# Performance work log

Measured on AMD Instinct MI355X. Metric: run time of the kernel, lower is better.

Reference implementation:

```python
import jax, jax.numpy as jnp
import numpy as np

NEG_SLOPE = 0.2  # GATConv default negative_slope


def gat_conv(x, row, col, W, b, a_src, a_dst, N):
    # GATConv, heads=1, flow='target_to_source': i=row (central), j=col (neighbor)
    h = x @ W                                                   # [N, C]
    e = jax.nn.leaky_relu((h @ a_src)[col] + (h @ a_dst)[row], NEG_SLOPE)  # [E]
    m = jax.ops.segment_max(e, row, num_segments=N)             # segment softmax over row
    w = jnp.exp(e - m[row])
    denom = jax.ops.segment_sum(w, row, num_segments=N)
    alpha = w / (denom[row] + 1e-16)
    out = jax.ops.segment_sum(alpha[:, None] * h[col], row, num_segments=N)
    return out + b


def lstm_scan(xs_t, Wih, Whh, bih, bhh):
    # xs_t: [L, N, C] -> hidden states [L, N, H]; PyTorch gate order i,f,g,o
    H = Whh.shape[1]
    Nn = xs_t.shape[1]
    bias = bih + bhh
    def step(carry, xt):
        h, c = carry
        g = xt @ Wih.T + h @ Whh.T + bias
        i, f, gg, o = jnp.split(g, 4, axis=-1)
        c = jax.nn.sigmoid(f) * c + jax.nn.sigmoid(i) * jnp.tanh(gg)
        h = jax.nn.sigmoid(o) * jnp.tanh(c)
        return (h, c), h
    init = (jnp.zeros((Nn, H), xs_t.dtype), jnp.zeros((Nn, H), xs_t.dtype))
    _, hs = jax.lax.scan(step, init, xs_t)
    return hs


def jk_lstm(xst, Wih_f, Whh_f, bih_f, bhh_f, Wih_b, Whh_b, bih_b, bhh_b, att_W, att_b):
    # xst: [L, N, C]; bidirectional LSTM over layer dim, attention-weighted sum
    hf = lstm_scan(xst, Wih_f, Whh_f, bih_f, bhh_f)
    hb = lstm_scan(xst[::-1], Wih_b, Whh_b, bih_b, bhh_b)[::-1]
    h = jnp.concatenate([hf, hb], axis=-1)                      # [L, N, 2H]
    score = jnp.einsum('lnh,h->ln', h, att_W) + att_b           # [L, N]
    alpha = jax.nn.softmax(score, axis=0)                       # softmax over layers
    return jnp.einsum('lnc,ln->nc', xst, alpha)                 # [N, C]


def setup_inputs() -> dict:
    key = jax.random.key(0)
    ks = list(jax.random.split(key, 32))
    N, E, C = 50000, 800000, 128
    L = 3
    H = (L * C) // 2  # 192; PyG JumpingKnowledge lstm hidden size
    s = 0.05
    d = {}
    d['x'] = jax.random.normal(ks[0], (N, 3), jnp.float32)
    d['edge_index'] = jax.random.randint(ks[1], (2, E), 0, N, jnp.int64)
    d['gat_W0'] = jax.random.normal(ks[2], (3, C)) * 0.3
    d['gat_b0'] = jnp.zeros((C,))
    d['gat_as0'] = jax.random.normal(ks[3], (C,)) * s
    d['gat_ad0'] = jax.random.normal(ks[4], (C,)) * s
    d['gat_W'] = jax.random.normal(ks[5], (L - 1, C, C)) * s
    d['gat_b'] = jnp.zeros((L - 1, C))
    d['gat_as'] = jax.random.normal(ks[6], (L - 1, C)) * s
    d['gat_ad'] = jax.random.normal(ks[7], (L - 1, C)) * s
    d['lstm_Wih_f'] = jax.random.normal(ks[8], (4 * H, C)) * s
    d['lstm_Whh_f'] = jax.random.normal(ks[9], (4 * H, H)) * s
    d['lstm_bih_f'] = jnp.zeros((4 * H,))
    d['lstm_bhh_f'] = jnp.zeros((4 * H,))
    d['lstm_Wih_b'] = jax.random.normal(ks[10], (4 * H, C)) * s
    d['lstm_Whh_b'] = jax.random.normal(ks[11], (4 * H, H)) * s
    d['lstm_bih_b'] = jnp.zeros((4 * H,))
    d['lstm_bhh_b'] = jnp.zeros((4 * H,))
    d['att_W'] = jax.random.normal(ks[12], (2 * H,)) * s
    d['att_b'] = jnp.zeros((1,))
    d['nW1'] = jax.random.normal(ks[13], (C, C)) * s
    d['nb1'] = jnp.zeros((C,))
    d['nW2'] = jax.random.normal(ks[14], (C, 2)) * s
    d['nb2'] = jnp.zeros((2,))
    d['eW1'] = jax.random.normal(ks[15], (2 * C, C)) * s
    d['eb1'] = jnp.zeros((C,))
    d['eW2'] = jax.random.normal(ks[16], (C, 2)) * s
    d['eb2'] = jnp.zeros((2,))
    return d


def reference(x, edge_index, gat_W0, gat_b0, gat_as0, gat_ad0, gat_W, gat_b, gat_as, gat_ad,
              lstm_Wih_f, lstm_Whh_f, lstm_bih_f, lstm_bhh_f,
              lstm_Wih_b, lstm_Whh_b, lstm_bih_b, lstm_bhh_b,
              att_W, att_b, nW1, nb1, nW2, nb2, eW1, eb1, eW2, eb2):
    N = x.shape[0]
    row, col = edge_index[0], edge_index[1]
    xs = []
    h = jax.nn.relu(gat_conv(x, row, col, gat_W0, gat_b0, gat_as0, gat_ad0, N))
    xs.append(h)
    for l in range(gat_W.shape[0]):  # fixed small layer count
        h = jax.nn.relu(gat_conv(h, row, col, gat_W[l], gat_b[l], gat_as[l], gat_ad[l], N))
        xs.append(h)
    xst = jnp.stack(xs, axis=0)  # [L, N, C]
    h = jk_lstm(xst, lstm_Wih_f, lstm_Whh_f, lstm_bih_f, lstm_bhh_f,
                lstm_Wih_b, lstm_Whh_b, lstm_bih_b, lstm_bhh_b, att_W, att_b)
    # node classifier (dropout is identity in eval)
    node_out = jax.nn.softmax(jax.nn.relu(h @ nW1 + nb1) @ nW2 + nb2, axis=1)
    # edge representation gather + concat, then edge classifier
    edge_rep = jnp.concatenate([h[row], h[col]], axis=1)  # [E, 2C]
    edge_out = jax.nn.softmax(jax.nn.relu(edge_rep @ eW1 + eb1) @ eW2 + eb2, axis=1)
    return node_out, edge_out
```

## Files before the change

kernel.cpp:

```cpp
#include <hip/hip_runtime.h>
#include <cstdint>
#include <cstddef>


#define NIN 28
#define MAXJOBS 20

struct InPtrs { const void* p[NIN]; int n[NIN]; };

struct PrepCfg {
    const void* src[MAXJOBS];
    float* dst[MAXJOBS];
    int n[MAXJOBS];
    int ai[MAXJOBS];
    int blk0[MAXJOBS + 1];
    int njobs;
    int cvB, wB, gB, tB;
    const void* esrc; int* row; int* col; int* cnt; int E;
    const void *Wihf, *Whhf, *Wihb, *Whhb, *bihf, *bhhf, *bihb, *bhhb;
    unsigned short* Bpack; float* bsum;
    const void* Wgsrc; unsigned short* Wg;
    const void* nW1src; const void* eW1src; unsigned short* Wt;
};

typedef short s16x4 __attribute__((ext_vector_type(4)));
typedef short s16x8 __attribute__((ext_vector_type(8)));
typedef float f32x4 __attribute__((ext_vector_type(4)));
typedef unsigned short u16x8 __attribute__((ext_vector_type(8)));

__device__ __forceinline__ float bf2f(unsigned short v) {
    unsigned int u = ((unsigned int)v) << 16;
    return __uint_as_float(u);
}

__device__ __forceinline__ unsigned short f2bf(float x) {
    unsigned int u = __float_as_uint(x);
    unsigned int r = u + 0x7fffu + ((u >> 16) & 1u);
    return (unsigned short)(r >> 16);
}

__device__ __forceinline__ float rdx(const void* p, size_t i, int isf32) {
    return isf32 ? ((const float*)p)[i] : bf2f(((const unsigned short*)p)[i]);
}

__device__ __forceinline__ float frcp(float x) {
    return __builtin_amdgcn_rcpf(x);
}

__device__ __forceinline__ float sigm(float x) {
    return frcp(1.f + __expf(-x));
}

__device__ __forceinline__ float fast_tanh(float x) {
    return 1.f - 2.f * frcp(__expf(2.f * x) + 1.f);
}

__global__ void k_sniff(InPtrs in, int* flags) {
    int ai = blockIdx.x;
    if (ai >= NIN) return;
    __shared__ int cnt;
    if (threadIdx.x == 0) cnt = 0;
    __syncthreads();
    if (ai == 1) {
        const int* w = (const int*)in.p[1];
        int nw = in.n[1] < 512 ? in.n[1] : 512;
        int local = 0;
        for (int i = threadIdx.x; i < nw; i += blockDim.x)
            if ((i & 1) && w[i] != 0) local++;
        atomicAdd(&cnt, local);
        __syncthreads();
        if (threadIdx.x == 0) flags[1] = (cnt < 4) ? 1 : 0;
        return;
    }
    const unsigned short* u = (const unsigned short*)in.p[ai];
    int ns = in.n[ai] < 256 ? in.n[ai] : 256;
    int local = 0;
    for (int i = threadIdx.x; i < ns; i += blockDim.x) {
        if (i & 1) continue;
        unsigned short v = u[i];
        int e = (v >> 7) & 0xff;
        if ((v & 0x7fff) != 0 && (e < 100 || e > 154)) local++;
    }
    atomicAdd(&cnt, local);
    __syncthreads();
    if (threadIdx.x == 0) flags[ai] = (cnt * 4 >= ns) ? 1 : 0;
}

__global__ void k_prep(PrepCfg C, const int* __restrict__ flags) {
    const int b = blockIdx.x;
    const int tid = threadIdx.x;
    if (b < C.cvB) {
        int j = 0;
        while (j + 1 < C.njobs && b >= C.blk0[j + 1]) ++j;
        int i = (b - C.blk0[j]) * 256 + tid;
        if (i < C.n[j]) C.dst[j][i] = rdx(C.src[j], i, flags[C.ai[j]]);
        return;
    }
    if (b < C.wB) {
        int i = (b - C.cvB) * 256 + tid;
        if (i >= C.E) return;
        int r, c;
        if (flags[1]) {
            const long long* s = (const long long*)C.esrc;
            r = (int)s[i];
            c = (int)s[(size_t)C.E + i];
        } else {
            const int* s = (const int*)C.esrc;
            r = s[i];
            c = s[(size_t)C.E + i];
        }
        C.row[i] = r;
        C.col[i] = c;
        atomicAdd(&C.cnt[r], 1);
        return;
    }
    if (b < C.gB) {
        int idx = (b - C.wB) * 256 + tid;
        const int TOT = 2 * 10 * 48 * 512;
        if (idx < TOT) {
            int dir = idx / (10 * 48 * 512);
            int r   = idx % (10 * 48 * 512);
            int kb  = r / (48 * 512);
            int r2  = r % (48 * 512);
            int f   = r2 / 512;
            int q   = r2 % 512;
            int lane = q >> 3, j = q & 7;
            int k   = kb * 32 + ((j >> 2) * 16) + ((lane >> 4) * 4) + (j & 3);
            int col = f * 16 + (lane & 15);
            float v;
            if (k < 128)
                v = dir ? rdx(C.Wihb, (size_t)col * 128 + k, flags[14])
                        : rdx(C.Wihf, (size_t)col * 128 + k, flags[10]);
            else
                v = dir ? rdx(C.Whhb, (size_t)col * 192 + (k - 128), flags[15])
                        : rdx(C.Whhf, (size_t)col * 192 + (k - 128), flags[11]);
            C.Bpack[idx] = f2bf(v);
        }
        if (idx < 2 * 768) {
            int d = idx / 768, j = idx % 768;
            C.bsum[idx] = d ? rdx(C.bihb, j, flags[16]) + rdx(C.bhhb, j, flags[17])
                            : rdx(C.bihf, j, flags[12]) + rdx(C.bhhf, j, flags[13]);
        }
        return;
    }
    if (b < C.tB) {
        int idx = (b - C.gB) * 256 + tid;
        if (idx >= 2 * 4 * 8 * 512) return;
        int layer = idx / 16384;
        int r  = idx % 16384;
        int kb = r / 4096;
        int r2 = r % 4096;
        int f  = r2 / 512;
        int q  = r2 % 512;
        int lane = q >> 3, j = q & 7;
        int k   = kb * 32 + ((j >> 2) * 16) + ((lane >> 4) * 4) + (j & 3);
        int col = f * 16 + (lane & 15);
        C.Wg[idx] = f2bf(rdx(C.Wgsrc, (size_t)layer * 16384 + (size_t)k * 128 + col,
                             flags[6]));
        return;
    }
    {
        int idx = (b - C.tB) * 256 + tid;
        if (idx >= 4 * 24 * 512) return;
        int kb = idx / (24 * 512);
        int r  = idx % (24 * 512);
        int fr = r / 512;
        int q  = r % 512;
        int lane = q >> 3, j = q & 7;
        int k   = kb * 32 + ((j >> 2) * 16) + ((lane >> 4) * 4) + (j & 3);
        int grp = fr >> 3;
        int col = (fr & 7) * 16 + (lane & 15);
        float v;
        if (grp == 0)      v = rdx(C.nW1src, (size_t)k * 128 + col, flags[20]);
        else if (grp == 1) v = rdx(C.eW1src, (size_t)k * 128 + col, flags[24]);
        else               v = rdx(C.eW1src, (size_t)(128 + k) * 128 + col, flags[24]);
        C.Wt[idx] = f2bf(v);
    }
}

__global__ void k_scan1(const int* __restrict__ deg, int* __restrict__ indptr,
                        int* __restrict__ bsums, int N) {
    __shared__ int buf[1024];
    const int t = threadIdx.x;
    const int base = blockIdx.x * 1024;
    int v = (base + t < N) ? deg[base + t] : 0;
    buf[t] = v;
    __syncthreads();
    for (int ofs = 1; ofs < 1024; ofs <<= 1) {
        int add = (t >= ofs) ? buf[t - ofs] : 0;
        __syncthreads();
        buf[t] += add;
        __syncthreads();
    }
    if (base + t < N) indptr[base + t] = buf[t] - v;
    if (t == 1023) bsums[blockIdx.x] = buf[1023];
}

__global__ void k_scan2(int* bsums, int nb) {
    if (threadIdx.x == 0 && blockIdx.x == 0) {
        int acc = 0;
        for (int j = 0; j < nb; ++j) { int v = bsums[j]; bsums[j] = acc; acc += v; }
        bsums[nb] = acc;
    }
}

__global__ void k_scan3(const int* __restrict__ bsums, int* __restrict__ indptr,
                        int* __restrict__ cnt, int N, int nb) {
    int i = blockIdx.x * blockDim.x + threadIdx.x;
    if (i < N) {
        indptr[i] += bsums[i >> 10];
        cnt[i] = 0;
    }
    if (i == 0) indptr[N] = bsums[nb];
}

__global__ void k_fill(const int* __restrict__ row, const int* __restrict__ col,
                       const int* __restrict__ indptr, int* __restrict__ cur,
                       int* __restrict__ colS, int* __restrict__ eidx, int E) {
    int i = blockIdx.x * blockDim.x + threadIdx.x;
    if (i >= E) return;
    int r = row[i];
    int p = indptr[r] + atomicAdd(&cur[r], 1);
    colS[p] = col[i];
    eidx[p] = i;
}

__global__ __launch_bounds__(256) void k_lin0(
    const float* __restrict__ x, const float* __restrict__ W0,
    const float* __restrict__ asrc, const float* __restrict__ adst,
    unsigned short* __restrict__ hlin, float* __restrict__ hs, float* __restrict__ hd,
    int N) {
    const int wid = threadIdx.x >> 6, lane = threadIdx.x & 63;
    const int n = blockIdx.x * 4 + wid;
    if (n >= N) return;
    float x0 = x[(size_t)n * 3], x1 = x[(size_t)n * 3 + 1], x2 = x[(size_t)n * 3 + 2];
    const int c0 = lane, c1 = lane + 64;
    float h0 = x0 * W0[c0] + x1 * W0[128 + c0] + x2 * W0[256 + c0];
    float h1 = x0 * W0[c1] + x1 * W0[128 + c1] + x2 * W0[256 + c1];
    hlin[(size_t)n * 128 + c0] = f2bf(h0);
    hlin[(size_t)n * 128 + c1] = f2bf(h1);
    float sp = h0 * asrc[c0] + h1 * asrc[c1];
    float dp = h0 * adst[c0] + h1 * adst[c1];
    for (int o = 32; o; o >>= 1) { sp += __shfl_down(sp, o); dp += __shfl_down(dp, o); }
    if (lane == 0) { hs[n] = sp; hd[n] = dp; }
}

__global__ __launch_bounds__(512) void k_linm(
    const unsigned short* __restrict__ xin,
    const unsigned short* __restrict__ Wg,
    const float* __restrict__ asrc, const float* __restrict__ adst,
    unsigned short* __restrict__ hlin, float* __restrict__ hs, float* __restrict__ hd,
    int N) {
    __shared__ unsigned short AS[64][136];
    __shared__ float hsS[64], hdS[64];
    const int t = threadIdx.x;
    const int f = t >> 6, lane = t & 63;
    const int n0 = blockIdx.x * 64;
    const int ccol = lane & 15;
    const int klane = lane >> 4;
    const int lrow = klane * 4;
    const int akl = klane * 4;
    const int m = f * 16 + ccol;

    const float asv = asrc[m], adv = adst[m];

    for (int i = t; i < 1024; i += 512) {
        int r = i >> 4, kq = (i & 15) * 8;
        u16x8 v = (u16x8)(0);
        if (n0 + r < N) v = *(const u16x8*)(xin + (size_t)(n0 + r) * 128 + kq);
        *(u16x8*)&AS[r][kq] = v;
    }
    if (t < 64) { hsS[t] = 0.f; hdS[t] = 0.f; }
    __syncthreads();

    f32x4 acc[4];
    #pragma unroll
    for (int rf = 0; rf < 4; ++rf) acc[rf] = (f32x4)(0.f);
    #pragma unroll
    for (int kb = 0; kb < 4; ++kb) {
        s16x8 b = *(const s16x8*)(Wg + ((size_t)kb * 8 + f) * 512 + lane * 8);
        const int k0 = kb * 32 + akl;
        #pragma unroll
        for (int rf = 0; rf < 4; ++rf) {
            s16x4 alo = *(const s16x4*)&AS[rf * 16 + ccol][k0];
            s16x4 ahi = *(const s16x4*)&AS[rf * 16 + ccol][k0 + 16];
            s16x8 av = __builtin_shufflevector(alo, ahi, 0, 1, 2, 3, 4, 5, 6, 7);
            acc[rf] = __builtin_amdgcn_mfma_f32_16x16x32_bf16(av, b, acc[rf], 0, 0, 0);
        }
    }
    __syncthreads();

    float sp[16], dp[16];
    #pragma unroll
    for (int rf = 0; rf < 4; ++rf) {
        #pragma unroll
        for (int reg = 0; reg < 4; ++reg) {
            float h = acc[rf][reg];
            int ci = rf * 4 + reg;
            AS[rf * 16 + lrow + reg][m] = f2bf(h);
            sp[ci] = h * asv;
            dp[ci] = h * adv;
        }
    }
    #pragma unroll
    for (int o = 1; o < 16; o <<= 1) {
        #pragma unroll
        for (int i = 0; i < 16; ++i) { sp[i] += __shfl_xor(sp[i], o); dp[i] += __shfl_xor(dp[i], o); }
    }
    if (ccol == 0) {
        #pragma unroll
        for (int i = 0; i < 16; ++i) {
            int row = (i >> 2) * 16 + lrow + (i & 3);
            atomicAdd(&hsS[row], sp[i]);
            atomicAdd(&hdS[row], dp[i]);
        }
    }
    __syncthreads();

    for (int i = t; i < 1024; i += 512) {
        int r = i >> 4, kq = (i & 15) * 8;
        if (n0 + r < N)
            *(u16x8*)(hlin + (size_t)(n0 + r) * 128 + kq) = *(const u16x8*)&AS[r][kq];
    }
    if (t < 64 && n0 + t < N) { hs[n0 + t] = hsS[t]; hd[n0 + t] = hdS[t]; }
}

__global__ __launch_bounds__(256) void k_aggr(
    const unsigned short* __restrict__ hlin, const float* __restrict__ hs,
    const float* __restrict__ hd,
    const int* __restrict__ indptr, const int* __restrict__ colS,
    const float* __restrict__ b, unsigned short* __restrict__ xout, int N) {
    const int wid = threadIdx.x >> 6, lane = threadIdx.x & 63;
    const int n = blockIdx.x * 4 + wid;
    if (n >= N) return;
    const int s = indptr[n], epos = indptr[n + 1];
    const float hdv = hd[n];
    const int c0 = lane * 2, c1 = lane * 2 + 1;
    float m = -1e30f, d = 0.f, a0 = 0.f, a1 = 0.f;
    int idx = s;
    for (; idx + 8 <= epos; idx += 8) {
        int cl[8];
        #pragma unroll
        for (int j = 0; j < 8; ++j) cl[j] = colS[idx + j];
        float e[8];
        #pragma unroll
        for (int j = 0; j < 8; ++j) {
            float ev = hs[cl[j]] + hdv;
            e[j] = (ev > 0.f) ? ev : 0.2f * ev;
        }
        unsigned int hw[8];
        #pragma unroll
        for (int j = 0; j < 8; ++j)
            hw[j] = *(const unsigned int*)(hlin + (size_t)cl[j] * 128 + c0);
        float m8 = e[0];
        #pragma unroll
        for (int j = 1; j < 8; ++j) m8 = fmaxf(m8, e[j]);
        if (m8 > m) {
            float sc = __expf(m - m8);
            a0 *= sc; a1 *= sc; d *= sc; m = m8;
        }
        #pragma unroll
        for (int j = 0; j < 8; ++j) {
            float w = __expf(e[j] - m);
            a0 += w * bf2f((unsigned short)(hw[j] & 0xffffu));
            a1 += w * bf2f((unsigned short)(hw[j] >> 16));
            d  += w;
        }
    }
    for (; idx < epos; ++idx) {
        int col = colS[idx];
        float e = hs[col] + hdv;
        e = (e > 0.f) ? e : 0.2f * e;
        unsigned int hw = *(const unsigned int*)(hlin + (size_t)col * 128 + c0);
        float v0 = bf2f((unsigned short)(hw & 0xffffu));
        float v1 = bf2f((unsigned short)(hw >> 16));
        if (e > m) {
            float sc = __expf(m - e);
            a0 = a0 * sc + v0;
            a1 = a1 * sc + v1;
            d  = d * sc + 1.f;
            m  = e;
        } else {
            float w = __expf(e - m);
            a0 += w * v0;
            a1 += w * v1;
            d  += w;
        }
    }
    float inv = frcp(d + 1e-16f);
    float r0 = a0 * inv + b[c0];
    float r1 = a1 * inv + b[c1];
    unsigned int ow = (unsigned int)f2bf(fmaxf(r0, 0.f))
                    | ((unsigned int)f2bf(fmaxf(r1, 0.f)) << 16);
    *(unsigned int*)(xout + (size_t)n * 128 + c0) = ow;
}

__global__ __launch_bounds__(768, 3) void k_lstm_mfma(
    const unsigned short* __restrict__ xsb,
    const unsigned short* __restrict__ Bpack,
    const float* __restrict__ bsum,
    const float* __restrict__ attW,
    float* __restrict__ scoreP,
    int N) {
    __shared__ unsigned short AS[64][332];
    __shared__ float scoreS[64];
    const int t = threadIdx.x;
    const int bf = t >> 6, lane = t & 63;
    const int dir = blockIdx.y;
    const int n0 = blockIdx.x * 64;
    const int ccol = lane & 15;
    const int klane = lane >> 4;
    const int lrow = klane * 4;
    const int akl = klane * 4;
    const int m = bf * 16 + ccol;

    const float bI = bsum[dir * 768 + m];
    const float bF = bsum[dir * 768 + 192 + m];
    const float bG = bsum[dir * 768 + 384 + m];
    const float bO = bsum[dir * 768 + 576 + m];
    const float awt = attW[dir * 192 + m];
    float cst[16];
    #pragma unroll
    for (int i = 0; i < 16; ++i) cst[i] = 0.f;

    const unsigned short* Bd = Bpack + (size_t)dir * 10 * 48 * 512;

    {
        const int l0 = dir ? 2 : 0;
        const unsigned short* xsrc = xsb + ((size_t)l0 * N + n0) * 128;
        for (int i = t; i < 1024; i += 768) {
            int r = i >> 4, kq = (i & 15) * 8;
            u16x8 v = (u16x8)(0);
            if (n0 + r < N) v = *(const u16x8*)(xsrc + (size_t)r * 128 + kq);
            *(u16x8*)&AS[r][kq] = v;
        }
    }
    if (t < 64) scoreS[t] = 0.f;
    __syncthreads();

    for (int s = 0; s < 3; ++s) {
        const int l = dir ? (2 - s) : s;

        const int KB = s ? 10 : 4;
        f32x4 acc[4][4];
        #pragma unroll
        for (int rf = 0; rf < 4; ++rf)
            #pragma unroll
            for (int g = 0; g < 4; ++g) acc[rf][g] = (f32x4)(0.f);
        s16x8 bA[4], bB[4];
        {
            const unsigned short* bb = Bd + (size_t)bf * 512 + lane * 8;
            #pragma unroll
            for (int g = 0; g < 4; ++g) bA[g] = *(const s16x8*)(bb + (size_t)g * 6144);
        }
        for (int kb = 0; kb < KB; kb += 2) {
            {
                const unsigned short* bb = Bd + ((size_t)(kb + 1) * 48 + bf) * 512 + lane * 8;
                #pragma unroll
                for (int g = 0; g < 4; ++g) bB[g] = *(const s16x8*)(bb + (size_t)g * 6144);
            }
            {
                const int k0 = kb * 32 + akl;
                s16x8 av[4];
                #pragma unroll
                for (int rf = 0; rf < 4; ++rf) {
                    s16x4 alo = *(const s16x4*)&AS[rf * 16 + ccol][k0];
                    s16x4 ahi = *(const s16x4*)&AS[rf * 16 + ccol][k0 + 16];
                    av[rf] = __builtin_shufflevector(alo, ahi, 0, 1, 2, 3, 4, 5, 6, 7);
                }
                #pragma unroll
                for (int rf = 0; rf < 4; ++rf)
                    #pragma unroll
                    for (int g = 0; g < 4; ++g)
                        acc[rf][g] = __builtin_amdgcn_mfma_f32_16x16x32_bf16(
                            av[rf], bA[g], acc[rf][g], 0, 0, 0);
            }
            if (kb + 2 < KB) {
                const unsigned short* bb = Bd + ((size_t)(kb + 2) * 48 + bf) * 512 + lane * 8;
                #pragma unroll
                for (int g = 0; g < 4; ++g) bA[g] = *(const s16x8*)(bb + (size_t)g * 6144);
            }
            {
                const int k0 = (kb + 1) * 32 + akl;
                s16x8 av[4];
                #pragma unroll
                for (int rf = 0; rf < 4; ++rf) {
                    s16x4 alo = *(const s16x4*)&AS[rf * 16 + ccol][k0];
                    s16x4 ahi = *(const s16x4*)&AS[rf * 16 + ccol][k0 + 16];
                    av[rf] = __builtin_shufflevector(alo, ahi, 0, 1, 2, 3, 4, 5, 6, 7);
                }
                #pragma unroll
                for (int rf = 0; rf < 4; ++rf)
                    #pragma unroll
                    for (int g = 0; g < 4; ++g)
                        acc[rf][g] = __builtin_amdgcn_mfma_f32_16x16x32_bf16(
                            av[rf], bB[g], acc[rf][g], 0, 0, 0);
            }
        }
        __syncthreads();

        u16x8 nx0 = (u16x8)(0), nx1 = (u16x8)(0);
        if (s < 2) {
            const int ln = dir ? (1 - s) : (s + 1);
            const unsigned short* xsrc = xsb + ((size_t)ln * N + n0) * 128;
            {
                int r = t >> 4, kq = (t & 15) * 8;
                if (n0 + r < N) nx0 = *(const u16x8*)(xsrc + (size_t)r * 128 + kq);
            }
            if (t < 256) {
                int i = t + 768, r = i >> 4, kq = (i & 15) * 8;
                if (n0 + r < N) nx1 = *(const u16x8*)(xsrc + (size_t)r * 128 + kq);
            }
        }

        float sp[16];
        #pragma unroll
        for (int rf = 0; rf < 4; ++rf) {
            #pragma unroll
            for (int reg = 0; reg < 4; ++reg) {
                float gI = acc[rf][0][reg] + bI;
                float gF = acc[rf][1][reg] + bF;
                float gG = acc[rf][2][reg] + bG;
                float gO = acc[rf][3][reg] + bO;
                float ig = sigm(gI);
                float fg = sigm(gF);
                float gt = fast_tanh(gG);
                float og = sigm(gO);
                int ci = rf * 4 + reg;
                float cn = fg * cst[ci] + ig * gt;
                cst[ci] = cn;
                float hh = og * fast_tanh(cn);
                AS[rf * 16 + lrow + reg][128 + m] = f2bf(hh);
                sp[ci] = hh * awt;
            }
        }
        #pragma unroll
        for (int o = 1; o < 16; o <<= 1) {
            #pragma unroll
            for (int i = 0; i < 16; ++i) sp[i] += __shfl_xor(sp[i], o);
        }
        if (ccol == 0) {
            #pragma unroll
            for (int i = 0; i < 16; ++i)
                atomicAdd(&scoreS[(i >> 2) * 16 + lrow + (i & 3)], sp[i]);
        }

        if (s < 2) {
            {
                int r = t >> 4, kq = (t & 15) * 8;
                *(u16x8*)&AS[r][kq] = nx0;
            }
            if (t < 256) {
                int i = t + 768, r = i >> 4, kq = (i & 15) * 8;
                *(u16x8*)&AS[r][kq] = nx1;
            }
        }
        __syncthreads();

        if (t < 64) {
            if (n0 + t < N)
                scoreP[(size_t)(dir * 3 + l) * N + n0 + t] = scoreS[t];
            scoreS[t] = 0.f;
        }
    }
}

__global__ __launch_bounds__(512) void k_tailm(
    const unsigned short* __restrict__ xsb, const float* __restrict__ scoreP,
    const unsigned short* __restrict__ Wt,
    const float* __restrict__ nb1, const float* __restrict__ nW2,
    const float* __restrict__ nb2, const float* __restrict__ eb1,
    unsigned short* __restrict__ P, unsigned short* __restrict__ Q,
    float* __restrict__ out, int N) {
    __shared__ unsigned short AS[64][136];
    __shared__ float al[64][4];
    __shared__ float lgt[64][2];
    const int t = threadIdx.x;
    const int f = t >> 6, lane = t & 63;
    const int n0 = blockIdx.x * 64;
    const int ccol = lane & 15;
    const int klane = lane >> 4;
    const int lrow = klane * 4;
    const int akl = klane * 4;
    const int m = f * 16 + ccol;

    if (t < 64) {
        int n = n0 + t;
        float e0 = 0.f, e1 = 0.f, e2 = 0.f;
        if (n < N) {
            float s0 = scoreP[n]                 + scoreP[(size_t)3 * N + n];
            float s1 = scoreP[(size_t)N + n]     + scoreP[(size_t)4 * N + n];
            float s2 = scoreP[(size_t)2 * N + n] + scoreP[(size_t)5 * N + n];
            float mm = fmaxf(s0, fmaxf(s1, s2));
            e0 = __expf(s0 - mm); e1 = __expf(s1 - mm); e2 = __expf(s2 - mm);
            float inv = frcp(e0 + e1 + e2);
            e0 *= inv; e1 *= inv; e2 *= inv;
        }
        al[t][0] = e0; al[t][1] = e1; al[t][2] = e2;
        lgt[t][0] = 0.f; lgt[t][1] = 0.f;
    }
    __syncthreads();

    const size_t L1o = (size_t)N * 128, L2o = 2 * L1o;
    for (int i = t; i < 1024; i += 512) {
        int r = i >> 4, kq = (i & 15) * 8;
        u16x8 o8 = (u16x8)(0);
        if (n0 + r < N) {
            size_t base = (size_t)(n0 + r) * 128 + kq;
            u16x8 a = *(const u16x8*)(xsb + base);
            u16x8 b = *(const u16x8*)(xsb + L1o + base);
            u16x8 c = *(const u16x8*)(xsb + L2o + base);
            float w0 = al[r][0], w1 = al[r][1], w2 = al[r][2];
            #pragma unroll
            for (int j = 0; j < 8; ++j)
                o8[j] = f2bf(w0 * bf2f(a[j]) + w1 * bf2f(b[j]) + w2 * bf2f(c[j]));
        }
        *(u16x8*)&AS[r][kq] = o8;
    }
    __syncthreads();

    f32x4 accN[4], accP[4], accQ[4];
    #pragma unroll
    for (int rf = 0; rf < 4; ++rf) { accN[rf] = (f32x4)(0.f); accP[rf] = (f32x4)(0.f); accQ[rf] = (f32x4)(0.f); }
    #pragma unroll
    for (int kb = 0; kb < 4; ++kb) {
        s16x8 bN = *(const s16x8*)(Wt + ((size_t)kb * 24 + f) * 512 + lane * 8);
        s16x8 bP = *(const s16x8*)(Wt + ((size_t)kb * 24 + 8 + f) * 512 + lane * 8);
        s16x8 bQ = *(const s16x8*)(Wt + ((size_t)kb * 24 + 16 + f) * 512 + lane * 8);
        const int k0 = kb * 32 + akl;
        #pragma unroll
        for (int rf = 0; rf < 4; ++rf) {
            s16x4 alo = *(const s16x4*)&AS[rf * 16 + ccol][k0];
            s16x4 ahi = *(const s16x4*)&AS[rf * 16 + ccol][k0 + 16];
            s16x8 av = __builtin_shufflevector(alo, ahi, 0, 1, 2, 3, 4, 5, 6, 7);
            accN[rf] = __builtin_amdgcn_mfma_f32_16x16x32_bf16(av, bN, accN[rf], 0, 0, 0);
            accP[rf] = __builtin_amdgcn_mfma_f32_16x16x32_bf16(av, bP, accP[rf], 0, 0, 0);
            accQ[rf] = __builtin_amdgcn_mfma_f32_16x16x32_bf16(av, bQ, accQ[rf], 0, 0, 0);
        }
    }
    __syncthreads();

    {
        const float nb1v = nb1[m];
        const float w20 = nW2[2 * m], w21 = nW2[2 * m + 1];
        float s0[16], s1[16];
        #pragma unroll
        for (int rf = 0; rf < 4; ++rf) {
            #pragma unroll
            for (int reg = 0; reg < 4; ++reg) {
                float h = fmaxf(accN[rf][reg] + nb1v, 0.f);
                int ci = rf * 4 + reg;
                s0[ci] = h * w20;
                s1[ci] = h * w21;
            }
        }
        #pragma unroll
        for (int o = 1; o < 16; o <<= 1) {
            #pragma unroll
            for (int i = 0; i < 16; ++i) { s0[i] += __shfl_xor(s0[i], o); s1[i] += __shfl_xor(s1[i], o); }
        }
        if (ccol == 0) {
            #pragma unroll
            for (int i = 0; i < 16; ++i) {
                int row = (i >> 2) * 16 + lrow + (i & 3);
                atomicAdd(&lgt[row][0], s0[i]);
                atomicAdd(&lgt[row][1], s1[i]);
            }
        }
    }
    {
        const float eb1v = eb1[m];
        #pragma unroll
        for (int rf = 0; rf < 4; ++rf)
            #pragma unroll
            for (int reg = 0; reg < 4; ++reg)
                AS[rf * 16 + lrow + reg][m] = f2bf(accP[rf][reg] + eb1v);
    }
    __syncthreads();
    if (t < 64 && n0 + t < N) {
        float l0 = lgt[t][0] + nb2[0], l1 = lgt[t][1] + nb2[1];
        float mm = fmaxf(l0, l1);
        float e0 = __expf(l0 - mm), e1 = __expf(l1 - mm);
        float inv = frcp(e0 + e1);
        out[2 * (size_t)(n0 + t)]     = e0 * inv;
        out[2 * (size_t)(n0 + t) + 1] = e1 * inv;
    }
    for (int i = t; i < 1024; i += 512) {
        int r = i >> 4, kq = (i & 15) * 8;
        if (n0 + r < N)
            *(u16x8*)(P + (size_t)(n0 + r) * 128 + kq) = *(const u16x8*)&AS[r][kq];
    }
    __syncthreads();
    #pragma unroll
    for (int rf = 0; rf < 4; ++rf)
        #pragma unroll
        for (int reg = 0; reg < 4; ++reg)
            AS[rf * 16 + lrow + reg][m] = f2bf(accQ[rf][reg]);
    __syncthreads();
    for (int i = t; i < 1024; i += 512) {
        int r = i >> 4, kq = (i & 15) * 8;
        if (n0 + r < N)
            *(u16x8*)(Q + (size_t)(n0 + r) * 128 + kq) = *(const u16x8*)&AS[r][kq];
    }
}

__global__ __launch_bounds__(256) void k_edge3(
    const unsigned short* __restrict__ P, const unsigned short* __restrict__ Q,
    const int* __restrict__ indptr, const int* __restrict__ colS,
    const int* __restrict__ eidx,
    const float* __restrict__ W2, const float* __restrict__ b2,
    float* __restrict__ out, int N) {
    const int wid = threadIdx.x >> 6, lane = threadIdx.x & 63;
    const int n = blockIdx.x * 4 + wid;
    if (n >= N) return;
    const int sl = lane & 15, g = lane >> 4;
    const int s = indptr[n], e = indptr[n + 1];
    float pf[8];
    {
        u16x8 pv = *(const u16x8*)(P + (size_t)n * 128 + sl * 8);
        #pragma unroll
        for (int j = 0; j < 8; ++j) pf[j] = bf2f(pv[j]);
    }
    const float* W2f = W2;
    const float b20 = b2[0], b21 = b2[1];
    for (int p = s + g; p < e; p += 8) {
        int p1 = p + 4;
        bool v1 = p1 < e;
        int col0 = colS[p],  eo0 = eidx[p];
        int col1 = v1 ? colS[p1] : col0;
        int eo1  = v1 ? eidx[p1] : 0;
        u16x8 qv0 = *(const u16x8*)(Q + (size_t)col0 * 128 + sl * 8);
        u16x8 qv1 = *(const u16x8*)(Q + (size_t)col1 * 128 + sl * 8);
        float l00 = 0.f, l01 = 0.f, l10 = 0.f, l11 = 0.f;
        #pragma unroll
        for (int j = 0; j < 8; ++j) {
            int ch = sl * 8 + j;
            float wA = W2f[ch * 2], wB = W2f[ch * 2 + 1];
            float h0 = fmaxf(pf[j] + bf2f(qv0[j]), 0.f);
            float h1 = fmaxf(pf[j] + bf2f(qv1[j]), 0.f);
            l00 += h0 * wA; l01 += h0 * wB;
            l10 += h1 * wA; l11 += h1 * wB;
        }
        #pragma unroll
        for (int o = 1; o < 16; o <<= 1) {
            l00 += __shfl_xor(l00, o); l01 += __shfl_xor(l01, o);
            l10 += __shfl_xor(l10, o); l11 += __shfl_xor(l11, o);
        }
        if (sl == 0) {
            {
                float a = l00 + b20, b = l01 + b21;
                float mm = fmaxf(a, b);
                float e0 = __expf(a - mm), e1 = __expf(b - mm);
                float inv = frcp(e0 + e1);
                out[2 * (size_t)N + 2 * (size_t)eo0]     = e0 * inv;
                out[2 * (size_t)N + 2 * (size_t)eo0 + 1] = e1 * inv;
            }
            if (v1) {
                float a = l10 + b20, b = l11 + b21;
                float mm = fmaxf(a, b);
                float e0 = __expf(a - mm), e1 = __expf(b - mm);
                float inv = frcp(e0 + e1);
                out[2 * (size_t)N + 2 * (size_t)eo1]     = e0 * inv;
                out[2 * (size_t)N + 2 * (size_t)eo1 + 1] = e1 * inv;
            }
        }
    }
}

extern "C" void kernel_launch(void* const* d_in, const int* in_sizes, int n_in,
                              void* d_out, int out_size, void* d_ws, size_t ws_size,
                              hipStream_t stream) {
    if (n_in < NIN) return;
    const int N = in_sizes[0] / 3;
    const int E = in_sizes[1] / 2;

    char* ws = (char*)d_ws;
    size_t off = 0;
    auto alloc = [&](size_t bytes) -> char* {
        char* p = ws + off;
        off = (off + bytes + 255) & ~(size_t)255;
        return p;
    };
    auto skipCanon = [](int i) {
        return i == 1 || (i >= 10 && i <= 17) || i == 6 || i == 20 || i == 24;
    };
    int* flags = (int*)alloc(32 * sizeof(int));
    int* bsums = (int*)alloc(128 * sizeof(int));
    float* canon[NIN];
    for (int i = 0; i < NIN; ++i) canon[i] = nullptr;
    for (int i = 0; i < NIN; ++i) {
        if (skipCanon(i)) continue;
        canon[i] = (float*)alloc((size_t)in_sizes[i] * 4);
    }
    int* row32  = (int*)alloc((size_t)E * 4);
    int* col32  = (int*)alloc((size_t)E * 4);
    int* indptr = (int*)alloc((size_t)(N + 1) * 4);
    int* cnt    = (int*)alloc((size_t)N * 4);
    int* colS   = (int*)alloc((size_t)E * 4);
    int* eidx   = (int*)alloc((size_t)E * 4);
    float* hs   = (float*)alloc((size_t)N * 4);
    float* hd   = (float*)alloc((size_t)N * 4);
    float* hJK  = (float*)alloc((size_t)N * 128 * 4);
    unsigned short* hlin = (unsigned short*)hJK;
    unsigned short* xsb = (unsigned short*)alloc((size_t)3 * N * 128 * 2);
    unsigned short* Bpack = (unsigned short*)alloc((size_t)2 * 10 * 48 * 512 * 2);
    unsigned short* Wg = (unsigned short*)alloc((size_t)2 * 4 * 8 * 512 * 2);
    unsigned short* Wt = (unsigned short*)alloc((size_t)4 * 24 * 512 * 2);
    float* bsum = (float*)alloc((size_t)2 * 768 * 4);
    float* scoreP = (float*)alloc((size_t)6 * N * 4);
    if (off > ws_size) return;
    unsigned short* P = (unsigned short*)hJK;
    unsigned short* Q = (unsigned short*)hJK + (size_t)N * 128;

    InPtrs ip;
    for (int i = 0; i < NIN; ++i) { ip.p[i] = d_in[i]; ip.n[i] = in_sizes[i]; }

    k_sniff<<<NIN, 256, 0, stream>>>(ip, flags);

    hipMemsetAsync(cnt, 0, (size_t)N * 4, stream);
    {
        PrepCfg C;
        int nj = 0, blk = 0;
        for (int i = 0; i < NIN; ++i) {
            if (skipCanon(i)) continue;
            C.src[nj] = d_in[i];
            C.dst[nj] = canon[i];
            C.n[nj] = in_sizes[i];
            C.ai[nj] = i;
            C.blk0[nj] = blk;
            blk += (in_sizes[i] + 255) / 256;
            ++nj;
        }
        C.blk0[nj] = blk;
        C.njobs = nj;
        C.cvB = blk;
        blk += (E + 255) / 256;                      C.wB = blk;
        blk += (2 * 10 * 48 * 512 + 255) / 256;      C.gB = blk;
        blk += (2 * 4 * 8 * 512 + 255) / 256;        C.tB = blk;
        blk += (4 * 24 * 512 + 255) / 256;
        C.esrc = d_in[1]; C.row = row32; C.col = col32; C.cnt = cnt; C.E = E;
        C.Wihf = d_in[10]; C.Whhf = d_in[11]; C.Wihb = d_in[14]; C.Whhb = d_in[15];
        C.bihf = d_in[12]; C.bhhf = d_in[13]; C.bihb = d_in[16]; C.bhhb = d_in[17];
        C.Bpack = Bpack; C.bsum = bsum;
        C.Wgsrc = d_in[6]; C.Wg = Wg;
        C.nW1src = d_in[20]; C.eW1src = d_in[24]; C.Wt = Wt;
        k_prep<<<blk, 256, 0, stream>>>(C, flags);
    }

    const int nb1k = (N + 1023) / 1024;
    k_scan1<<<nb1k, 1024, 0, stream>>>(cnt, indptr, bsums, N);
    k_scan2<<<1, 64, 0, stream>>>(bsums, nb1k);
    k_scan3<<<(N + 255) / 256, 256, 0, stream>>>(bsums, indptr, cnt, N, nb1k);
    k_fill<<<(E + 255) / 256, 256, 0, stream>>>(row32, col32, indptr, cnt, colS, eidx, E);

    k_lin0<<<(N + 3) / 4, 256, 0, stream>>>(canon[0], canon[2], canon[4], canon[5],
                                            hlin, hs, hd, N);
    k_aggr<<<(N + 3) / 4, 256, 0, stream>>>(hlin, hs, hd, indptr, colS, canon[3], xsb, N);
    for (int l = 1; l < 3; ++l) {
        const unsigned short* Wgl = Wg + (size_t)(l - 1) * 4 * 8 * 512;
        const float* bb = canon[7] + (size_t)(l - 1) * 128;
        const float* as = canon[8] + (size_t)(l - 1) * 128;
        const float* ad = canon[9] + (size_t)(l - 1) * 128;
        k_linm<<<(N + 63) / 64, 512, 0, stream>>>(xsb + (size_t)(l - 1) * N * 128, Wgl,
                                                  as, ad, hlin, hs, hd, N);
        k_aggr<<<(N + 3) / 4, 256, 0, stream>>>(hlin, hs, hd, indptr, colS, bb,
                                                xsb + (size_t)l * N * 128, N);
    }

    dim3 lgrid((N + 63) / 64, 2);
    k_lstm_mfma<<<lgrid, 768, 0, stream>>>(xsb, Bpack, bsum, canon[18], scoreP, N);

    float* out = (float*)d_out;
    k_tailm<<<(N + 63) / 64, 512, 0, stream>>>(xsb, scoreP, Wt,
                                               canon[21], canon[22], canon[23], canon[25],
                                               P, Q, out, N);
    k_edge3<<<(N + 3) / 4, 256, 0, stream>>>(P, Q, indptr, colS, eidx,
                                             canon[26], canon[27], out, N);
}
```

Baseline: 583.7 us.

## Fuse small launches into prep kernels and unroll edge classifier loop

Folds the cnt memset into the sniff kernel, merges the first-layer linear transform into the prep kernel, and folds the serial block-sum scan into each scan3 block via a shared-memory scan. This removes several kernel launches and one single-thread kernel. The edge-classifier tail now processes four edges per iteration instead of two, giving more gathers in flight at the cost of more registers.

```diff
diff --git a/kernel.cpp b/kernel.cpp
--- a/kernel.cpp
+++ b/kernel.cpp
@@ -15,12 +15,14 @@
     int ai[MAXJOBS];
     int blk0[MAXJOBS + 1];
     int njobs;
-    int cvB, wB, gB, tB;
+    int cvB, wB, gB, tB, l0B;
     const void* esrc; int* row; int* col; int* cnt; int E;
     const void *Wihf, *Whhf, *Wihb, *Whhb, *bihf, *bhhf, *bihb, *bhhb;
     unsigned short* Bpack; float* bsum;
     const void* Wgsrc; unsigned short* Wg;
     const void* nW1src; const void* eW1src; unsigned short* Wt;
+    const void *xsrc0, *W0src, *as0src, *ad0src;
+    unsigned short* hlin; float* hs; float* hd; int N;
 };
 
 typedef short s16x4 __attribute__((ext_vector_type(4)));
@@ -55,9 +57,13 @@
     return 1.f - 2.f * frcp(__expf(2.f * x) + 1.f);
 }
 
-__global__ void k_sniff(InPtrs in, int* flags) {
+__global__ void k_sniff(InPtrs in, int* flags, int* cntz, int N) {
     int ai = blockIdx.x;
-    if (ai >= NIN) return;
+    if (ai >= NIN) {
+        int i = (ai - NIN) * 256 + threadIdx.x;
+        if (i < N) cntz[i] = 0;
+        return;
+    }
     __shared__ int cnt;
     if (threadIdx.x == 0) cnt = 0;
     __syncthreads();
@@ -159,7 +165,7 @@
                              flags[6]));
         return;
     }
-    {
+    if (b < C.l0B) {
         int idx = (b - C.tB) * 256 + tid;
         if (idx >= 4 * 24 * 512) return;
         int kb = idx / (24 * 512);
@@ -175,6 +181,27 @@
         else if (grp == 1) v = rdx(C.eW1src, (size_t)k * 128 + col, flags[24]);
         else               v = rdx(C.eW1src, (size_t)(128 + k) * 128 + col, flags[24]);
         C.Wt[idx] = f2bf(v);
+        return;
+    }
+    {
+        const int wid = tid >> 6, lane = tid & 63;
+        const int n = (b - C.l0B) * 4 + wid;
+        if (n >= C.N) return;
+        const int f32x = flags[0], f32w = flags[2];
+        float x0 = rdx(C.xsrc0, (size_t)n * 3 + 0, f32x);
+        float x1 = rdx(C.xsrc0, (size_t)n * 3 + 1, f32x);
+        float x2 = rdx(C.xsrc0, (size_t)n * 3 + 2, f32x);
+        const int c0 = lane, c1 = lane + 64;
+        float h0 = x0 * rdx(C.W0src, c0, f32w) + x1 * rdx(C.W0src, 128 + c0, f32w)
+                 + x2 * rdx(C.W0src, 256 + c0, f32w);
+        float h1 = x0 * rdx(C.W0src, c1, f32w) + x1 * rdx(C.W0src, 128 + c1, f32w)
+                 + x2 * rdx(C.W0src, 256 + c1, f32w);
+        C.hlin[(size_t)n * 128 + c0] = f2bf(h0);
+        C.hlin[(size_t)n * 128 + c1] = f2bf(h1);
+        float sp = h0 * rdx(C.as0src, c0, flags[4]) + h1 * rdx(C.as0src, c1, flags[4]);
+        float dp = h0 * rdx(C.ad0src, c0, flags[5]) + h1 * rdx(C.ad0src, c1, flags[5]);
+        for (int o = 32; o; o >>= 1) { sp += __shfl_down(sp, o); dp += __shfl_down(dp, o); }
+        if (lane == 0) { C.hs[n] = sp; C.hd[n] = dp; }
     }
 }
 
@@ -196,22 +223,37 @@
     if (t == 1023) bsums[blockIdx.x] = buf[1023];
 }
 
-__global__ void k_scan2(int* bsums, int nb) {
-    if (threadIdx.x == 0 && blockIdx.x == 0) {
-        int acc = 0;
-        for (int j = 0; j < nb; ++j) { int v = bsums[j]; bsums[j] = acc; acc += v; }
-        bsums[nb] = acc;
-    }
-}
-
 __global__ void k_scan3(const int* __restrict__ bsums, int* __restrict__ indptr,
                         int* __restrict__ cnt, int N, int nb) {
-    int i = blockIdx.x * blockDim.x + threadIdx.x;
+    __shared__ int buf[256];
+    __shared__ int sh[258];
+    const int t = threadIdx.x;
+    if (nb <= 256) {
+        int v = (t < nb) ? bsums[t] : 0;
+        buf[t] = v;
+        __syncthreads();
+        for (int ofs = 1; ofs < 256; ofs <<= 1) {
+            int add = (t >= ofs) ? buf[t - ofs] : 0;
+            __syncthreads();
+            buf[t] += add;
+            __syncthreads();
+        }
+        if (t < nb) sh[t] = buf[t] - v;
+        if (t == 0) sh[nb] = buf[255];
+    } else {
+        if (t == 0) {
+            int acc = 0;
+            for (int j = 0; j < nb && j < 257; ++j) { sh[j] = acc; acc += bsums[j]; }
+            sh[nb < 257 ? nb : 257] = acc;
+        }
+    }
+    __syncthreads();
+    int i = blockIdx.x * blockDim.x + t;
     if (i < N) {
-        indptr[i] += bsums[i >> 10];
+        indptr[i] += sh[i >> 10];
         cnt[i] = 0;
     }
-    if (i == 0) indptr[N] = bsums[nb];
+    if (i == 0) indptr[N] = sh[nb];
 }
 
 __global__ void k_fill(const int* __restrict__ row, const int* __restrict__ col,
@@ -223,26 +265,6 @@
     int p = indptr[r] + atomicAdd(&cur[r], 1);
     colS[p] = col[i];
     eidx[p] = i;
-}
-
-__global__ __launch_bounds__(256) void k_lin0(
-    const float* __restrict__ x, const float* __restrict__ W0,
-    const float* __restrict__ asrc, const float* __restrict__ adst,
-    unsigned short* __restrict__ hlin, float* __restrict__ hs, float* __restrict__ hd,
-    int N) {
-    const int wid = threadIdx.x >> 6, lane = threadIdx.x & 63;
-    const int n = blockIdx.x * 4 + wid;
-    if (n >= N) return;
-    float x0 = x[(size_t)n * 3], x1 = x[(size_t)n * 3 + 1], x2 = x[(size_t)n * 3 + 2];
-    const int c0 = lane, c1 = lane + 64;
-    float h0 = x0 * W0[c0] + x1 * W0[128 + c0] + x2 * W0[256 + c0];
-    float h1 = x0 * W0[c1] + x1 * W0[128 + c1] + x2 * W0[256 + c1];
-    hlin[(size_t)n * 128 + c0] = f2bf(h0);
-    hlin[(size_t)n * 128 + c1] = f2bf(h1);
-    float sp = h0 * asrc[c0] + h1 * asrc[c1];
-    float dp = h0 * adst[c0] + h1 * adst[c1];
-    for (int o = 32; o; o >>= 1) { sp += __shfl_down(sp, o); dp += __shfl_down(dp, o); }
-    if (lane == 0) { hs[n] = sp; hd[n] = dp; }
 }
 
 __global__ __launch_bounds__(512) void k_linm(
@@ -723,45 +745,51 @@
     }
     const float* W2f = W2;
     const float b20 = b2[0], b21 = b2[1];
-    for (int p = s + g; p < e; p += 8) {
-        int p1 = p + 4;
-        bool v1 = p1 < e;
-        int col0 = colS[p],  eo0 = eidx[p];
-        int col1 = v1 ? colS[p1] : col0;
-        int eo1  = v1 ? eidx[p1] : 0;
-        u16x8 qv0 = *(const u16x8*)(Q + (size_t)col0 * 128 + sl * 8);
-        u16x8 qv1 = *(const u16x8*)(Q + (size_t)col1 * 128 + sl * 8);
-        float l00 = 0.f, l01 = 0.f, l10 = 0.f, l11 = 0.f;
+    for (int p = s + g; p < e; p += 16) {
+        int pp[4];
+        bool vv[4];
+        int col[4], eo[4];
+        #pragma unroll
+        for (int k = 0; k < 4; ++k) {
+            pp[k] = p + 4 * k;
+            vv[k] = pp[k] < e;
+            col[k] = vv[k] ? colS[pp[k]] : colS[p];
+            eo[k]  = vv[k] ? eidx[pp[k]] : 0;
+        }
+        u16x8 qv[4];
+        #pragma unroll
+        for (int k = 0; k < 4; ++k)
+            qv[k] = *(const u16x8*)(Q + (size_t)col[k] * 128 + sl * 8);
+        float l0[4] = {0.f, 0.f, 0.f, 0.f}, l1[4] = {0.f, 0.f, 0.f, 0.f};
         #pragma unroll
         for (int j = 0; j < 8; ++j) {
             int ch = sl * 8 + j;
             float wA = W2f[ch * 2], wB = W2f[ch * 2 + 1];
-            float h0 = fmaxf(pf[j] + bf2f(qv0[j]), 0.f);
-            float h1 = fmaxf(pf[j] + bf2f(qv1[j]), 0.f);
-            l00 += h0 * wA; l01 += h0 * wB;
-            l10 += h1 * wA; l11 += h1 * wB;
+            #pragma unroll
+            for (int k = 0; k < 4; ++k) {
+                float h = fmaxf(pf[j] + bf2f(qv[k][j]), 0.f);
+                l0[k] += h * wA;
+                l1[k] += h * wB;
+            }
         }
         #pragma unroll
         for (int o = 1; o < 16; o <<= 1) {
-            l00 += __shfl_xor(l00, o); l01 += __shfl_xor(l01, o);
-            l10 += __shfl_xor(l10, o); l11 += __shfl_xor(l11, o);
+            #pragma unroll
+            for (int k = 0; k < 4; ++k) {
+                l0[k] += __shfl_xor(l0[k], o);
+                l1[k] += __shfl_xor(l1[k], o);
+            }
         }
         if (sl == 0) {
-            {
-                float a = l00 + b20, b = l01 + b21;
-                float mm = fmaxf(a, b);
-                float e0 = __expf(a - mm), e1 = __expf(b - mm);
+            #pragma unroll
+            for (int k = 0; k < 4; ++k) {
+                if (!vv[k]) continue;
+                float a = l0[k] + b20, bq = l1[k] + b21;
+                float mm = fmaxf(a, bq);
+                float e0 = __expf(a - mm), e1 = __expf(bq - mm);
                 float inv = frcp(e0 + e1);
-                out[2 * (size_t)N + 2 * (size_t)eo0]     = e0 * inv;
-                out[2 * (size_t)N + 2 * (size_t)eo0 + 1] = e1 * inv;
-            }
-            if (v1) {
-                float a = l10 + b20, b = l11 + b21;
-                float mm = fmaxf(a, b);
-                float e0 = __expf(a - mm), e1 = __expf(b - mm);
-                float inv = frcp(e0 + e1);
-                out[2 * (size_t)N + 2 * (size_t)eo1]     = e0 * inv;
-                out[2 * (size_t)N + 2 * (size_t)eo1 + 1] = e1 * inv;
+                out[2 * (size_t)N + 2 * (size_t)eo[k]]     = e0 * inv;
+                out[2 * (size_t)N + 2 * (size_t)eo[k] + 1] = e1 * inv;
             }
         }
     }
@@ -782,7 +810,8 @@
         return p;
     };
     auto skipCanon = [](int i) {
-        return i == 1 || (i >= 10 && i <= 17) || i == 6 || i == 20 || i == 24;
+        return i == 0 || i == 1 || i == 2 || i == 4 || i == 5 ||
+               (i >= 10 && i <= 17) || i == 6 || i == 20 || i == 24;
     };
     int* flags = (int*)alloc(32 * sizeof(int));
     int* bsums = (int*)alloc(128 * sizeof(int));
@@ -815,9 +844,8 @@
     InPtrs ip;
     for (int i = 0; i < NIN; ++i) { ip.p[i] = d_in[i]; ip.n[i] = in_sizes[i]; }
 
-    k_sniff<<<NIN, 256, 0, stream>>>(ip, flags);
-
-    hipMemsetAsync(cnt, 0, (size_t)N * 4, stream);
+    k_sniff<<<NIN + (N + 255) / 256, 256, 0, stream>>>(ip, flags, cnt, N);
+
     {
         PrepCfg C;
         int nj = 0, blk = 0;
@@ -837,24 +865,24 @@
         blk += (E + 255) / 256;                      C.wB = blk;
         blk += (2 * 10 * 48 * 512 + 255) / 256;      C.gB = blk;
         blk += (2 * 4 * 8 * 512 + 255) / 256;        C.tB = blk;
-        blk += (4 * 24 * 512 + 255) / 256;
+        blk += (4 * 24 * 512 + 255) / 256;           C.l0B = blk;
+        blk += (N + 3) / 4;
         C.esrc = d_in[1]; C.row = row32; C.col = col32; C.cnt = cnt; C.E = E;
         C.Wihf = d_in[10]; C.Whhf = d_in[11]; C.Wihb = d_in[14]; C.Whhb = d_in[15];
         C.bihf = d_in[12]; C.bhhf = d_in[13]; C.bihb = d_in[16]; C.bhhb = d_in[17];
         C.Bpack = Bpack; C.bsum = bsum;
         C.Wgsrc = d_in[6]; C.Wg = Wg;
         C.nW1src = d_in[20]; C.eW1src = d_in[24]; C.Wt = Wt;
+        C.xsrc0 = d_in[0]; C.W0src = d_in[2]; C.as0src = d_in[4]; C.ad0src = d_in[5];
+        C.hlin = hlin; C.hs = hs; C.hd = hd; C.N = N;
         k_prep<<<blk, 256, 0, stream>>>(C, flags);
     }
 
     const int nb1k = (N + 1023) / 1024;
     k_scan1<<<nb1k, 1024, 0, stream>>>(cnt, indptr, bsums, N);
-    k_scan2<<<1, 64, 0, stream>>>(bsums, nb1k);
     k_scan3<<<(N + 255) / 256, 256, 0, stream>>>(bsums, indptr, cnt, N, nb1k);
     k_fill<<<(E + 255) / 256, 256, 0, stream>>>(row32, col32, indptr, cnt, colS, eidx, E);
 
-    k_lin0<<<(N + 3) / 4, 256, 0, stream>>>(canon[0], canon[2], canon[4], canon[5],
-                                            hlin, hs, hd, N);
     k_aggr<<<(N + 3) / 4, 256, 0, stream>>>(hlin, hs, hd, indptr, colS, canon[3], xsb, N);
     for (int l = 1; l < 3; ++l) {
         const unsigned short* Wgl = Wg + (size_t)(l - 1) * 4 * 8 * 512;
```

Measured after the change: 577.4 us. About the same (-1.1%).
